# Performance work log

Hardware: AMD Instinct MI355X
Metric: run time of the kernel (lower is better)

## Reference

```python
import jax, jax.numpy as jnp
import numpy as np

NUM_CLASSES = 10
P_CUTOFF = 0.95
TEMP = 0.5  # temperature used throughout the original forward
B_LB, B_ULB, D = 4096, 6144, 128


def _l2_normalize(x, eps=1e-12):
    # matches torch.nn.functional.normalize(x, dim=1)
    n = jnp.linalg.norm(x, axis=1, keepdims=True)
    return x / jnp.maximum(n, eps)


def setup_inputs() -> dict:
    key = jax.random.key(0)
    k = jax.random.split(key, 6)
    anchor_feat = jax.random.normal(k[0], (B_ULB, D), jnp.float32)
    positive_feat = jax.random.normal(k[1], (B_ULB, D), jnp.float32)
    lb_feat = jax.random.normal(k[2], (B_LB, D), jnp.float32)
    labels = jax.random.randint(k[3], (B_LB,), 0, NUM_CLASSES)
    lb_one_hot = jax.nn.one_hot(labels, NUM_CLASSES, dtype=jnp.float32)
    # scale logits so a realistic fraction of unlabeled samples pass the 0.95 cutoff
    logits_x_ulb_1 = 3.0 * jax.random.normal(k[4], (B_ULB, NUM_CLASSES), jnp.float32)
    logits_x_ulb_2 = 3.0 * jax.random.normal(k[5], (B_ULB, NUM_CLASSES), jnp.float32)
    return {
        "anchor_feat": anchor_feat,
        "positive_feat": positive_feat,
        "lb_feat": lb_feat,
        "lb_one_hot": lb_one_hot,
        "logits_x_ulb_1": logits_x_ulb_1,
        "logits_x_ulb_2": logits_x_ulb_2,
    }


def reference(anchor_feat, positive_feat, lb_feat, lb_one_hot,
              logits_x_ulb_1, logits_x_ulb_2):
    # pick the more-confident view per unlabeled sample
    prob1 = jax.nn.softmax(logits_x_ulb_1 / TEMP, axis=1)
    prob2 = jax.nn.softmax(logits_x_ulb_2 / TEMP, axis=1)
    take1 = jnp.max(prob1, axis=-1) >= jnp.max(prob2, axis=-1)
    logits_gt = jnp.where(take1[:, None], logits_x_ulb_1, logits_x_ulb_2)

    # confidence mask at p_cutoff = 0.95
    mask = (jax.nn.softmax(logits_gt, axis=1) >= P_CUTOFF).astype(logits_gt.dtype)
    logits_gt = logits_gt * mask

    # per-class counts: labeled via one-hot sum; unlabeled via vectorized bincount
    class_num_lb = lb_one_hot.sum(axis=0)
    max_val = jnp.max(logits_gt, axis=1)
    max_idx = jnp.argmax(logits_gt, axis=1)
    valid = (max_val != 0).astype(jnp.float32)  # max_val==0 -> idx -1 -> skipped
    class_num_ulb = jnp.zeros((NUM_CLASSES,), jnp.float32).at[max_idx].add(valid) * 2.0
    class_num = class_num_ulb + class_num_lb

    # build [B_lb + 2*B_ulb, 10] target distribution
    logits_x_ulb = jnp.concatenate([logits_gt, logits_gt], axis=0)
    prob_xulb = jax.nn.softmax(logits_x_ulb / TEMP, axis=-1)
    logits_bf = jnp.concatenate([lb_one_hot, prob_xulb], axis=0)  # [N, 10]

    # self-attention over normalized features (second normalize in the original
    # is idempotent on already unit-norm rows)
    feats = _l2_normalize(jnp.concatenate([lb_feat, anchor_feat, positive_feat], axis=0))  # [N, D]
    attn = jax.nn.softmax(feats @ feats.T / TEMP, axis=1)  # [N, N]
    self_atten = attn @ logits_bf  # [N, 10]

    # per-class division; zero-count classes divided by total count
    denom = jnp.where(class_num == 0, class_num.sum(), class_num)
    logits_af = self_atten / denom[None, :]
    return logits_af
```

## Files before the change

kernel.cpp:

```cpp
#include <hip/hip_runtime.h>
#include <hip/hip_bf16.h>

#define NLB 4096
#define NULB 6144
#define NROWS 16384
#define DD 128
#define NC 10
#define VW 12
#define SEG 16
#define JSEG (NROWS / SEG)
#define NTILE (JSEG / 64)
#define BI 256
#define BJ 64
#define NVB 256
#define SQRTC 1.6986437f

typedef __bf16 bf16_t;
typedef _Float16 f16_t;
typedef f16_t f16x8 __attribute__((ext_vector_type(8)));
typedef float f32x4 __attribute__((ext_vector_type(4)));
typedef short i16x2 __attribute__((ext_vector_type(2)));
typedef int i32x8 __attribute__((ext_vector_type(8)));
typedef unsigned int u32;
typedef unsigned char u8;

__device__ __forceinline__ size_t f8idx(int row, int c) {
  return ((size_t)(row >> 7) << 14) + (size_t)((row & 127) << 7)
       + (size_t)(((c ^ (row & 7)) & 7) << 4);
}

__device__ __forceinline__ u32 packexp2f16(float c0, float c1) {
#if __has_builtin(__builtin_amdgcn_cvt_pknorm_i16)
  float y0 = fmaf(c0, 1.2207465e-4f, 0.46740490f);
  float y1 = fmaf(c1, 1.2207465e-4f, 0.46740490f);
  union { i16x2 p; u32 u; } cv;
  cv.p = __builtin_amdgcn_cvt_pknorm_i16(y0, y1);
  return cv.u;
#else
  u32 b0 = (u32)(int)fmaf(c0, 4.0f, 15315.354f);
  u32 b1 = (u32)(int)fmaf(c1, 4.0f, 15315.354f);
  return __builtin_amdgcn_perm(b1, b0, 0x05040100u);
#endif
}

__global__ void kprep2(const float* __restrict__ lb, const float* __restrict__ an,
                       const float* __restrict__ po, const float* __restrict__ onehot,
                       const float* __restrict__ l1, const float* __restrict__ l2,
                       u8* __restrict__ F8, f16_t* __restrict__ VF,
                       float* __restrict__ clsPart) {
  __shared__ float Vtmp[64 * 16];
  __shared__ float lcnt[NC];
  int b = blockIdx.x;
  int t = threadIdx.x;

  if (b < 1024) {
    int row = b * 16 + (t >> 4);
    int c = t & 15;
    const float* src;
    if (row < NLB) src = lb + (size_t)row * DD;
    else if (row < NLB + NULB) src = an + (size_t)(row - NLB) * DD;
    else src = po + (size_t)(row - NLB - NULB) * DD;
    float4 v0 = ((const float4*)src)[c * 2];
    float4 v1 = ((const float4*)src)[c * 2 + 1];
    float ss = v0.x*v0.x + v0.y*v0.y + v0.z*v0.z + v0.w*v0.w
             + v1.x*v1.x + v1.y*v1.y + v1.z*v1.z + v1.w*v1.w;
#pragma unroll
    for (int off = 8; off >= 1; off >>= 1) ss += __shfl_xor(ss, off);
    float inv = (16.0f * SQRTC) / fmaxf(sqrtf(ss), 1e-12f);
    u32 d0 = (u32)__builtin_amdgcn_cvt_pk_fp8_f32(v0.x*inv, v0.y*inv, 0, false);
    d0 = (u32)__builtin_amdgcn_cvt_pk_fp8_f32(v0.z*inv, v0.w*inv, d0, true);
    u32 d1 = (u32)__builtin_amdgcn_cvt_pk_fp8_f32(v1.x*inv, v1.y*inv, 0, false);
    d1 = (u32)__builtin_amdgcn_cvt_pk_fp8_f32(v1.z*inv, v1.w*inv, d1, true);
    uint2 dd = {d0, d1};
    *(uint2*)(F8 + f8idx(row, c >> 1) + ((c & 1) << 3)) = dd;
    return;
  }

  int vb = b - 1024;
  if (t < NC) lcnt[t] = 0.0f;
  __syncthreads();
  if (t < 64) {
    int gid = vb * 64 + t;
    float p[16];
    p[10] = 1.0f; p[11] = 0.f; p[12] = 0.f; p[13] = 0.f; p[14] = 0.f; p[15] = 0.f;
    if (gid < NLB) {
      int idx = 0;
#pragma unroll
      for (int c = 0; c < NC; ++c) {
        p[c] = onehot[(size_t)gid * NC + c];
        if (p[c] == 1.0f) idx = c;
      }
      atomicAdd(&lcnt[idx], 1.0f);
    } else {
      int r = (gid < NLB + NULB) ? (gid - NLB) : (gid - NLB - NULB);
      bool count = (gid < NLB + NULB);
      float a[NC], bb[NC];
#pragma unroll
      for (int c = 0; c < NC; ++c) { a[c] = l1[(size_t)r * NC + c]; bb[c] = l2[(size_t)r * NC + c]; }
      float m1 = a[0], m2 = bb[0];
#pragma unroll
      for (int c = 1; c < NC; ++c) { m1 = fmaxf(m1, a[c]); m2 = fmaxf(m2, bb[c]); }
      float s1 = 0.0f, s2 = 0.0f;
#pragma unroll
      for (int c = 0; c < NC; ++c) {
        s1 += expf(2.0f * (a[c] - m1));
        s2 += expf(2.0f * (bb[c] - m2));
      }
      bool take1 = (s1 <= s2);
      float g[NC];
#pragma unroll
      for (int c = 0; c < NC; ++c) g[c] = take1 ? a[c] : bb[c];
      float mg = g[0];
#pragma unroll
      for (int c = 1; c < NC; ++c) mg = fmaxf(mg, g[c]);
      float e[NC]; float sg = 0.0f;
#pragma unroll
      for (int c = 0; c < NC; ++c) { e[c] = expf(g[c] - mg); sg += e[c]; }
      float msk[NC];
#pragma unroll
      for (int c = 0; c < NC; ++c) msk[c] = ((e[c] / sg) >= 0.95f) ? g[c] : 0.0f;
      float mx = msk[0]; int mi = 0;
#pragma unroll
      for (int c = 1; c < NC; ++c) if (msk[c] > mx) { mx = msk[c]; mi = c; }
      if (count && mx != 0.0f) atomicAdd(&lcnt[mi], 2.0f);
      float mm = 2.0f * msk[0];
#pragma unroll
      for (int c = 1; c < NC; ++c) mm = fmaxf(mm, 2.0f * msk[c]);
      float q[NC]; float sp = 0.0f;
#pragma unroll
      for (int c = 0; c < NC; ++c) { q[c] = expf(2.0f * msk[c] - mm); sp += q[c]; }
#pragma unroll
      for (int c = 0; c < NC; ++c) p[c] = q[c] / sp;
    }
#pragma unroll
    for (int c = 0; c < 16; ++c) Vtmp[t * 16 + c] = p[c];
  }
  __syncthreads();
  if (t < 16) clsPart[(size_t)vb * 16 + t] = (t < NC) ? lcnt[t] : 0.0f;
  if (t < 128) {
    int gbase = vb * 2;
    int G = t >> 6;
    int l = t & 63;
    int q = l >> 4;
    int n = l & 15;
    union { f16_t h[8]; uint4 uu; } pk;
#pragma unroll
    for (int d = 0; d < 4; ++d) {
      pk.h[d]     = (f16_t)Vtmp[(G * 32      + q * 4 + d) * 16 + n];
      pk.h[4 + d] = (f16_t)Vtmp[(G * 32 + 16 + q * 4 + d) * 16 + n];
    }
    *(uint4*)(VF + ((size_t)(gbase + G) * 64 + l) * 8) = pk.uu;
  }
}

__launch_bounds__(256, 4)
__global__ void kattn(const u8* __restrict__ F8, const f16_t* __restrict__ VF,
                      float* __restrict__ Ppart) {
  __shared__ __align__(16) u8 Fs[2][BJ * 128];
  __shared__ uint4 Vs4[2][128];
  int t = threadIdx.x;
  int lane = t & 63;
  int wave = t >> 6;
  int q = lane >> 4;
  int r = lane & 15;
  int i0 = blockIdx.x * BI + wave * 64;
  int jbase = blockIdx.y * JSEG;

  i32x8 bfr[4];
#pragma unroll
  for (int s = 0; s < 4; ++s) {
    int row = i0 + s * 16 + r;
    union { uint4 h[2]; i32x8 v; } bb;
    bb.h[0] = *(const uint4*)(F8 + f8idx(row, 2 * q));
    bb.h[1] = *(const uint4*)(F8 + f8idx(row, 2 * q + 1));
    bfr[s] = bb.v;
  }

  f32x4 acc[4];
#pragma unroll
  for (int s = 0; s < 4; ++s) acc[s] = (f32x4){0.f, 0.f, 0.f, 0.f};
  const f32x4 kZero = {0.f, 0.f, 0.f, 0.f};

  auto stage = [&](int buf, int j0) {
    const uint4* srcF = (const uint4*)(F8 + (((size_t)(j0 >> 7)) << 14)
                                          + (((size_t)(j0 & 64)) << 7));
#pragma unroll
    for (int k = 0; k < 2; ++k) {
      int off = (k << 8) + t;
      __builtin_amdgcn_global_load_lds(
          (const __attribute__((address_space(1))) uint4*)(srcF + off),
          (__attribute__((address_space(3))) uint4*)((uint4*)Fs[buf] + off), 16, 0, 0);
    }
    if (t < 128) {
      const uint4* srcV = (const uint4*)VF + ((size_t)(j0 >> 5) << 6);
      __builtin_amdgcn_global_load_lds(
          (const __attribute__((address_space(1))) uint4*)(srcV + t),
          (__attribute__((address_space(3))) uint4*)(Vs4[buf] + t), 16, 0, 0);
    }
  };

  auto compute = [&](int buf) {
    const u8* fsb = Fs[buf];
    const uint4* vsb = Vs4[buf];
#pragma unroll
    for (int jp = 0; jp < 2; ++jp) {
      union { uint4 h[2]; i32x8 v; } afe, afo;
      const u8* re = fsb + (jp * 32 + r) * 128;
      const u8* ro = re + 16 * 128;
      int c0 = (((2 * q) ^ (r & 7)) & 7) << 4;
      int c1 = (((2 * q + 1) ^ (r & 7)) & 7) << 4;
      afe.h[0] = *(const uint4*)(re + c0);
      afe.h[1] = *(const uint4*)(re + c1);
      afo.h[0] = *(const uint4*)(ro + c0);
      afo.h[1] = *(const uint4*)(ro + c1);
      union { uint4 qd; f16x8 v; } bv;
      bv.qd = vsb[jp * 64 + lane];

      __builtin_amdgcn_s_setprio(1);
      f32x4 ce = __builtin_amdgcn_mfma_scale_f32_16x16x128_f8f6f4(
          afe.v, bfr[0], kZero, 0, 0, 0, 0x7F7F7F7Fu, 0, 0x7F7F7F7Fu);
      f32x4 co = __builtin_amdgcn_mfma_scale_f32_16x16x128_f8f6f4(
          afo.v, bfr[0], kZero, 0, 0, 0, 0x7F7F7F7Fu, 0, 0x7F7F7F7Fu);
      __builtin_amdgcn_s_setprio(0);
#pragma unroll
      for (int s = 0; s < 4; ++s) {
        f32x4 cen, con;
        if (s < 3) {
          __builtin_amdgcn_s_setprio(1);
          cen = __builtin_amdgcn_mfma_scale_f32_16x16x128_f8f6f4(
              afe.v, bfr[s + 1], kZero, 0, 0, 0, 0x7F7F7F7Fu, 0, 0x7F7F7F7Fu);
          con = __builtin_amdgcn_mfma_scale_f32_16x16x128_f8f6f4(
              afo.v, bfr[s + 1], kZero, 0, 0, 0, 0x7F7F7F7Fu, 0, 0x7F7F7F7Fu);
          __builtin_amdgcn_s_setprio(0);
        }
        union { u32 u[4]; f16x8 v; } pf;
        pf.u[0] = packexp2f16(ce[0], ce[1]);
        pf.u[1] = packexp2f16(ce[2], ce[3]);
        pf.u[2] = packexp2f16(co[0], co[1]);
        pf.u[3] = packexp2f16(co[2], co[3]);
        __builtin_amdgcn_s_setprio(1);
        acc[s] = __builtin_amdgcn_mfma_f32_16x16x32_f16(pf.v, bv.v, acc[s], 0, 0, 0);
        __builtin_amdgcn_s_setprio(0);
        if (s < 3) { ce = cen; co = con; }
      }
    }
  };

  stage(0, jbase);
  __syncthreads();
#pragma unroll
  for (int jt = 0; jt < NTILE - 1; ++jt) {
    stage((jt + 1) & 1, jbase + (jt + 1) * BJ);
    compute(jt & 1);
    __syncthreads();
  }
  compute((NTILE - 1) & 1);

  if (r < 12) {
    float* base = Ppart + ((size_t)blockIdx.y * NROWS + (size_t)i0) * VW;
#pragma unroll
    for (int s = 0; s < 4; ++s) {
      float* op = base + (s * 16 + q * 4) * VW + r;
      op[0 * VW] = acc[s][0];
      op[1 * VW] = acc[s][1];
      op[2 * VW] = acc[s][2];
      op[3 * VW] = acc[s][3];
    }
  }
}

__global__ void kfinal(float* __restrict__ out, const float* __restrict__ Ppart,
                       const float* __restrict__ clsPart) {
  __shared__ float clsS[16];
  int t = threadIdx.x;
  const float4* cp = (const float4*)clsPart;
  float4 c0 = {0.f, 0.f, 0.f, 0.f}, c1 = c0;
  float c2x = 0.f, c2y = 0.f;
#pragma unroll
  for (int k = 0; k < 4; ++k) {
    int rr = t + 64 * k;
    float4 x0 = cp[rr * 4], x1 = cp[rr * 4 + 1], x2 = cp[rr * 4 + 2];
    c0.x += x0.x; c0.y += x0.y; c0.z += x0.z; c0.w += x0.w;
    c1.x += x1.x; c1.y += x1.y; c1.z += x1.z; c1.w += x1.w;
    c2x += x2.x; c2y += x2.y;
  }
#pragma unroll
  for (int off = 32; off >= 1; off >>= 1) {
    c0.x += __shfl_xor(c0.x, off); c0.y += __shfl_xor(c0.y, off);
    c0.z += __shfl_xor(c0.z, off); c0.w += __shfl_xor(c0.w, off);
    c1.x += __shfl_xor(c1.x, off); c1.y += __shfl_xor(c1.y, off);
    c1.z += __shfl_xor(c1.z, off); c1.w += __shfl_xor(c1.w, off);
    c2x += __shfl_xor(c2x, off); c2y += __shfl_xor(c2y, off);
  }
  if (t == 0) {
    *(float4*)&clsS[0] = c0;
    *(float4*)&clsS[4] = c1;
    clsS[8] = c2x; clsS[9] = c2y;
    clsS[10] = 0.f; clsS[11] = 0.f; clsS[12] = 0.f;
    clsS[13] = 0.f; clsS[14] = 0.f; clsS[15] = 0.f;
  }
  __syncthreads();
  float d[NC]; float tot = 0.0f;
#pragma unroll
  for (int c = 0; c < NC; ++c) { d[c] = clsS[c]; tot += d[c]; }

  int row = blockIdx.x * 64 + t;
  float4 a0 = {0.f, 0.f, 0.f, 0.f}, a1 = a0, a2 = a0;
#pragma unroll
  for (int s = 0; s < SEG; ++s) {
    const float4* pr = (const float4*)(Ppart + ((size_t)s * NROWS + (size_t)row) * VW);
    float4 x0 = pr[0], x1 = pr[1], x2 = pr[2];
    a0.x += x0.x; a0.y += x0.y; a0.z += x0.z; a0.w += x0.w;
    a1.x += x1.x; a1.y += x1.y; a1.z += x1.z; a1.w += x1.w;
    a2.x += x2.x; a2.y += x2.y; a2.z += x2.z;
  }
  float num[NC] = {a0.x, a0.y, a0.z, a0.w, a1.x, a1.y, a1.z, a1.w, a2.x, a2.y};
  float rs = 1.0f / a2.z;
  float* op = out + (size_t)row * NC;
#pragma unroll
  for (int c = 0; c < NC; ++c) {
    float den = (d[c] == 0.0f) ? tot : d[c];
    op[c] = num[c] * rs / den;
  }
}

extern "C" void kernel_launch(void* const* d_in, const int* in_sizes, int n_in,
                              void* d_out, int out_size, void* d_ws, size_t ws_size,
                              hipStream_t stream) {
  const float* anchor   = (const float*)d_in[0];
  const float* positive = (const float*)d_in[1];
  const float* lbfeat   = (const float*)d_in[2];
  const float* onehot   = (const float*)d_in[3];
  const float* l1       = (const float*)d_in[4];
  const float* l2       = (const float*)d_in[5];
  float* out = (float*)d_out;

  char* ws = (char*)d_ws;
  u8*     F8      = (u8*)ws;
  f16_t*  VF      = (f16_t*)(ws + 2097152);
  float*  Ppart   = (float*)(ws + 2097152 + 524288);
  float*  clsPart = (float*)(ws + 2097152 + 524288 + (size_t)SEG * NROWS * VW * 4);

  kprep2<<<1024 + NVB, 256, 0, stream>>>(lbfeat, anchor, positive, onehot, l1, l2,
                                         F8, VF, clsPart);
  kattn<<<dim3(NROWS / BI, SEG), 256, 0, stream>>>(F8, VF, Ppart);
  kfinal<<<NVB, 64, 0, stream>>>(out, Ppart, clsPart);
}
```

Measured before the change: 112.7 us.

## Replace LDS double-buffered staging with direct register-prefetched global loads

The attention kernel no longer stages key features and value fragments through shared memory with global_load_lds and barriers. Each wave now loads its own fp8 key fragments and f16 value fragments straight from global memory into registers, prefetching one 32-column group ahead of compute, with no __syncthreads. The MFMA software pipelining inside compute is also simplified. This removes LDS traffic and block-wide synchronisation, but every wave now fetches the same key data independently, raising global/L2 load traffic and register pressure.

```diff
diff --git a/kernel.cpp b/kernel.cpp
--- a/kernel.cpp
+++ b/kernel.cpp
@@ -9,9 +9,7 @@
 #define VW 12
 #define SEG 16
 #define JSEG (NROWS / SEG)
-#define NTILE (JSEG / 64)
 #define BI 256
-#define BJ 64
 #define NVB 256
 #define SQRTC 1.6986437f
 
@@ -156,8 +154,6 @@
 __launch_bounds__(256, 4)
 __global__ void kattn(const u8* __restrict__ F8, const f16_t* __restrict__ VF,
                       float* __restrict__ Ppart) {
-  __shared__ __align__(16) u8 Fs[2][BJ * 128];
-  __shared__ uint4 Vs4[2][128];
   int t = threadIdx.x;
   int lane = t & 63;
   int wave = t >> 6;
@@ -181,80 +177,54 @@
   for (int s = 0; s < 4; ++s) acc[s] = (f32x4){0.f, 0.f, 0.f, 0.f};
   const f32x4 kZero = {0.f, 0.f, 0.f, 0.f};
 
-  auto stage = [&](int buf, int j0) {
-    const uint4* srcF = (const uint4*)(F8 + (((size_t)(j0 >> 7)) << 14)
-                                          + (((size_t)(j0 & 64)) << 7));
-#pragma unroll
-    for (int k = 0; k < 2; ++k) {
-      int off = (k << 8) + t;
-      __builtin_amdgcn_global_load_lds(
-          (const __attribute__((address_space(1))) uint4*)(srcF + off),
-          (__attribute__((address_space(3))) uint4*)((uint4*)Fs[buf] + off), 16, 0, 0);
-    }
-    if (t < 128) {
-      const uint4* srcV = (const uint4*)VF + ((size_t)(j0 >> 5) << 6);
-      __builtin_amdgcn_global_load_lds(
-          (const __attribute__((address_space(1))) uint4*)(srcV + t),
-          (__attribute__((address_space(3))) uint4*)(Vs4[buf] + t), 16, 0, 0);
+  struct Frag { uint4 e0, e1, o0, o1, v; };
+
+  auto loadfr = [&](int jpg) -> Frag {
+    Frag f;
+    int je = jbase + jpg * 32 + r;
+    int jo = je + 16;
+    f.e0 = *(const uint4*)(F8 + f8idx(je, 2 * q));
+    f.e1 = *(const uint4*)(F8 + f8idx(je, 2 * q + 1));
+    f.o0 = *(const uint4*)(F8 + f8idx(jo, 2 * q));
+    f.o1 = *(const uint4*)(F8 + f8idx(jo, 2 * q + 1));
+    f.v  = *((const uint4*)VF + ((size_t)(jbase >> 5) + jpg) * 64 + lane);
+    return f;
+  };
+
+  auto compute = [&](const Frag& f) {
+    union { uint4 h[2]; i32x8 v; } afe, afo;
+    afe.h[0] = f.e0; afe.h[1] = f.e1;
+    afo.h[0] = f.o0; afo.h[1] = f.o1;
+    union { uint4 qd; f16x8 v; } bv;
+    bv.qd = f.v;
+#pragma unroll
+    for (int s = 0; s < 4; ++s) {
+      __builtin_amdgcn_s_setprio(1);
+      f32x4 ce = __builtin_amdgcn_mfma_scale_f32_16x16x128_f8f6f4(
+          afe.v, bfr[s], kZero, 0, 0, 0, 0x7F7F7F7Fu, 0, 0x7F7F7F7Fu);
+      f32x4 co = __builtin_amdgcn_mfma_scale_f32_16x16x128_f8f6f4(
+          afo.v, bfr[s], kZero, 0, 0, 0, 0x7F7F7F7Fu, 0, 0x7F7F7F7Fu);
+      __builtin_amdgcn_s_setprio(0);
+      union { u32 u[4]; f16x8 v; } pf;
+      pf.u[0] = packexp2f16(ce[0], ce[1]);
+      pf.u[1] = packexp2f16(ce[2], ce[3]);
+      pf.u[2] = packexp2f16(co[0], co[1]);
+      pf.u[3] = packexp2f16(co[2], co[3]);
+      __builtin_amdgcn_s_setprio(1);
+      acc[s] = __builtin_amdgcn_mfma_f32_16x16x32_f16(pf.v, bv.v, acc[s], 0, 0, 0);
+      __builtin_amdgcn_s_setprio(0);
     }
   };
 
-  auto compute = [&](int buf) {
-    const u8* fsb = Fs[buf];
-    const uint4* vsb = Vs4[buf];
-#pragma unroll
-    for (int jp = 0; jp < 2; ++jp) {
-      union { uint4 h[2]; i32x8 v; } afe, afo;
-      const u8* re = fsb + (jp * 32 + r) * 128;
-      const u8* ro = re + 16 * 128;
-      int c0 = (((2 * q) ^ (r & 7)) & 7) << 4;
-      int c1 = (((2 * q + 1) ^ (r & 7)) & 7) << 4;
-      afe.h[0] = *(const uint4*)(re + c0);
-      afe.h[1] = *(const uint4*)(re + c1);
-      afo.h[0] = *(const uint4*)(ro + c0);
-      afo.h[1] = *(const uint4*)(ro + c1);
-      union { uint4 qd; f16x8 v; } bv;
-      bv.qd = vsb[jp * 64 + lane];
-
-      __builtin_amdgcn_s_setprio(1);
-      f32x4 ce = __builtin_amdgcn_mfma_scale_f32_16x16x128_f8f6f4(
-          afe.v, bfr[0], kZero, 0, 0, 0, 0x7F7F7F7Fu, 0, 0x7F7F7F7Fu);
-      f32x4 co = __builtin_amdgcn_mfma_scale_f32_16x16x128_f8f6f4(
-          afo.v, bfr[0], kZero, 0, 0, 0, 0x7F7F7F7Fu, 0, 0x7F7F7F7Fu);
-      __builtin_amdgcn_s_setprio(0);
-#pragma unroll
-      for (int s = 0; s < 4; ++s) {
-        f32x4 cen, con;
-        if (s < 3) {
-          __builtin_amdgcn_s_setprio(1);
-          cen = __builtin_amdgcn_mfma_scale_f32_16x16x128_f8f6f4(
-              afe.v, bfr[s + 1], kZero, 0, 0, 0, 0x7F7F7F7Fu, 0, 0x7F7F7F7Fu);
-          con = __builtin_amdgcn_mfma_scale_f32_16x16x128_f8f6f4(
-              afo.v, bfr[s + 1], kZero, 0, 0, 0, 0x7F7F7F7Fu, 0, 0x7F7F7F7Fu);
-          __builtin_amdgcn_s_setprio(0);
-        }
-        union { u32 u[4]; f16x8 v; } pf;
-        pf.u[0] = packexp2f16(ce[0], ce[1]);
-        pf.u[1] = packexp2f16(ce[2], ce[3]);
-        pf.u[2] = packexp2f16(co[0], co[1]);
-        pf.u[3] = packexp2f16(co[2], co[3]);
-        __builtin_amdgcn_s_setprio(1);
-        acc[s] = __builtin_amdgcn_mfma_f32_16x16x32_f16(pf.v, bv.v, acc[s], 0, 0, 0);
-        __builtin_amdgcn_s_setprio(0);
-        if (s < 3) { ce = cen; co = con; }
-      }
-    }
-  };
-
-  stage(0, jbase);
-  __syncthreads();
-#pragma unroll
-  for (int jt = 0; jt < NTILE - 1; ++jt) {
-    stage((jt + 1) & 1, jbase + (jt + 1) * BJ);
-    compute(jt & 1);
-    __syncthreads();
-  }
-  compute((NTILE - 1) & 1);
+  const int NJP = JSEG / 32;
+  Frag cur = loadfr(0);
+#pragma unroll 2
+  for (int jpg = 0; jpg < NJP - 1; ++jpg) {
+    Frag nxt = loadfr(jpg + 1);
+    compute(cur);
+    cur = nxt;
+  }
+  compute(cur);
 
   if (r < 12) {
     float* base = Ppart + ((size_t)blockIdx.y * NROWS + (size_t)i0) * VW;
```

Measured after the change: 113.0 us. No clear change (+0.3%).
